# Optimization experiments

Hardware: AMD Instinct MI355X
Metric: run time of the kernel (lower is better)

## Reference

```python
import jax, jax.numpy as jnp
import numpy as np

THRESH = 8000.0  # saturating partial-sum accumulator threshold (thresh=8000 in source)
GROUP = 128      # channel chunk size used by split_tensor_* helpers
EPS = 1e-5

def binarize(x):
    # sign() forward with straight-through estimator (standard BinarizeConv2d behavior)
    return x + jax.lax.stop_gradient(jnp.sign(x) - x)

def psum_conv3x3(x, w):
    """3x3 'same' conv computed as 9 shifted-window partial sums per 128-channel
    group, with the running accumulator saturated to [-THRESH, THRESH] after each
    partial sum (emulating a low-bit hardware accumulator).
    x: [B, C, H, W]; w: [O, C, 3, 3] -> out [B, O, H, W]."""
    B, C, H, W = x.shape
    O = w.shape[0]
    xp = jnp.pad(x, ((0, 0), (0, 0), (1, 1), (1, 1)))
    acc = jnp.zeros((B, O, H, W), dtype=x.dtype)
    n_groups = C // GROUP
    for g in range(n_groups):
        xg = xp[:, g * GROUP:(g + 1) * GROUP]
        wg = w[:, g * GROUP:(g + 1) * GROUP]
        # split_tensor ordering: x1..x9 vary row (dim2) fastest, then col (dim3)
        for col in range(3):
            for row in range(3):
                part = jnp.einsum('bchw,oc->bohw',
                                  xg[:, :, row:row + H, col:col + W],
                                  wg[:, :, row, col])
                acc = jnp.clip(acc + part, -THRESH, THRESH)
    return acc

def batchnorm(x, gamma, beta, mean, var):
    inv = gamma / jnp.sqrt(var + EPS)
    return x * inv[None, :, None, None] + (beta - mean * inv)[None, :, None, None]

def setup_inputs() -> dict:
    key = jax.random.key(0)
    ks = jax.random.split(key, 12)
    B, C, H, W = 64, 128, 56, 56
    return {
        'x': jax.random.normal(ks[0], (B, C, H, W), jnp.float32),
        'w1': jax.random.normal(ks[1], (C, C, 3, 3), jnp.float32),
        'w2': jax.random.normal(ks[2], (C, C, 3, 3), jnp.float32),
        'gamma1': jax.random.uniform(ks[3], (C,), jnp.float32, 0.5, 1.5),
        'beta1': jax.random.normal(ks[4], (C,), jnp.float32) * 0.1,
        'mean1': jax.random.normal(ks[5], (C,), jnp.float32),
        'var1': jax.random.uniform(ks[6], (C,), jnp.float32, 0.5, 1.5),
        'gamma2': jax.random.uniform(ks[7], (C,), jnp.float32, 0.5, 1.5),
        'beta2': jax.random.normal(ks[8], (C,), jnp.float32) * 0.1,
        'mean2': jax.random.normal(ks[9], (C,), jnp.float32),
        'var2': jax.random.uniform(ks[10], (C,), jnp.float32, 0.5, 1.5),
    }

def reference(x, w1, w2, gamma1, beta1, mean1, var1, gamma2, beta2, mean2, var2):
    residual = x
    out = psum_conv3x3(binarize(x), binarize(w1))
    out = batchnorm(out, gamma1, beta1, mean1, var1)
    out = jnp.clip(out, -1.0, 1.0)  # hardtanh
    out = psum_conv3x3(binarize(out), binarize(w2))
    out = batchnorm(out, gamma2, beta2, mean2, var2)
    out = out + residual
    out = jnp.clip(out, -1.0, 1.0)
    return out
```

## Files before the change

### kernel.cpp

```cpp
#include <hip/hip_runtime.h>
#include <cstdint>
#include <cstddef>


typedef int      v4i __attribute__((ext_vector_type(4)));
typedef float    v4f __attribute__((ext_vector_type(4)));

constexpr int B = 64, C = 128, H = 56, W = 56;
constexpr int HP = H + 2, WP = W + 2;
constexpr int PIX = H * W;
constexpr int M = B * H * W;
constexpr int NTILES = M / 256;
constexpr int TPX = NTILES / 8;

constexpr size_t XS_BYTES = (size_t)B * HP * WP * C;
constexpr size_t XS1_OFF = 0;
constexpr size_t XS2_OFF = XS_BYTES;
constexpr size_t WF_BYTES = 18 * 8192;
constexpr size_t WF1_OFF = 2 * XS_BYTES;
constexpr size_t WF2_OFF = WF1_OFF + WF_BYTES;
constexpr size_t BNP_OFF = WF2_OFF + WF_BYTES;

__global__ __launch_bounds__(256) void zero_halo(int8_t* __restrict__ xs1,
                                                 int8_t* __restrict__ xs2) {
    int b = blockIdx.x >> 2;
    int q = blockIdx.x & 3;
    int t = q * 256 + threadIdx.x;
    size_t ib = (size_t)b * HP * WP * C;
#pragma unroll
    for (int a = 0; a < 2; ++a) {
        uint32_t* p = (uint32_t*)((a ? xs2 : xs1) + ib);
        const int ROWD = WP * C / 4;
        for (int i = t; i < ROWD; i += 1024) {
            p[i] = 0;
            p[(HP - 1) * ROWD + i] = 0;
        }
        for (int i = t; i < 56 * 2 * 32; i += 1024) {
            int r = i >> 6;
            int side = (i >> 5) & 1;
            int j = i & 31;
            p[((r + 1) * WP + side * (WP - 1)) * (C / 4) + j] = 0;
        }
    }
}

__global__ __launch_bounds__(256) void prep_x(const float* __restrict__ x,
                                              int8_t* __restrict__ xs) {
    __shared__ uint32_t tl[256 * 33];
    int t = threadIdx.x;
    int m = blockIdx.x * 256 + t;
    int b_ = m / PIX, hw = m % PIX;
    const float* xp = x + (size_t)b_ * C * PIX + hw;
#pragma unroll
    for (int c4 = 0; c4 < 32; ++c4) {
        uint32_t v = 0;
#pragma unroll
        for (int j = 0; j < 4; ++j) {
            float f = xp[(size_t)(c4 * 4 + j) * PIX];
            v |= ((uint32_t)(uint8_t)(int8_t)((f > 0.f) - (f < 0.f))) << (8 * j);
        }
        tl[t * 33 + c4] = v;
    }
    __syncthreads();
    int pl = t >> 3, co = t & 7;
#pragma unroll
    for (int pass = 0; pass < 8; ++pass) {
        int p = pass * 32 + pl;
        int mg = blockIdx.x * 256 + p;
        int b2 = mg / PIX, hw2 = mg % PIX, h2 = hw2 / W, w2 = hw2 % W;
        size_t ob = ((size_t)(b2 * HP + h2 + 1) * WP + (w2 + 1)) * C + co * 16;
        v4i val;
#pragma unroll
        for (int k = 0; k < 4; ++k) val[k] = (int)tl[p * 33 + co * 4 + k];
        *(v4i*)(xs + ob) = val;
    }
}

__global__ __launch_bounds__(256) void prep_w(
    const float* __restrict__ w1, const float* __restrict__ w2,
    const float* __restrict__ g1, const float* __restrict__ be1,
    const float* __restrict__ mu1, const float* __restrict__ va1,
    const float* __restrict__ g2, const float* __restrict__ be2,
    const float* __restrict__ mu2, const float* __restrict__ va2,
    int8_t* __restrict__ wf1, int8_t* __restrict__ wf2,
    float* __restrict__ bnp) {
    int t = blockIdx.x * 256 + threadIdx.x;
    if (t < 256) {
        int o = t & 127;
        if (t < 128) {
            float inv = g1[o] / sqrtf(va1[o] + 1e-5f);
            bnp[o]       = inv;
            bnp[128 + o] = __fsub_rn(be1[o], __fmul_rn(mu1[o], inv));
        } else {
            float inv = g2[o] / sqrtf(va2[o] + 1e-5f);
            bnp[256 + o] = inv;
            bnp[384 + o] = __fsub_rn(be2[o], __fmul_rn(mu2[o], inv));
        }
    }
    if (t >= 2 * 18 * 8 * 64) return;
    int lane = t & 63;
    int j    = (t >> 6) & 7;
    int kh   = (t >> 9) & 1;
    int tap  = (t >> 10) % 9;
    int which = (t >> 10) / 9;
    const float* w = which ? w2 : w1;
    int8_t* wf = which ? wf2 : wf1;
    int o = (j >> 2) * 64 + (lane & 15) * 4 + (j & 3);
    int cbase = kh * 64 + (lane >> 4) * 16;
    int r = tap / 3, s = tap % 3;
    int8_t frag[16];
#pragma unroll
    for (int jj = 0; jj < 16; ++jj) {
        float f = w[((size_t)(o * C + cbase + jj) * 3 + r) * 3 + s];
        frag[jj] = (int8_t)((f > 0.f) - (f < 0.f));
    }
    *(v4i*)(wf + (size_t)(((tap * 2 + kh) * 8 + j) * 64 + lane) * 16) =
        *(const v4i*)frag;
}

template <int PHASE>
__global__ __launch_bounds__(512, 1) void conv_bin(
    const int8_t* __restrict__ xs,
    const int8_t* __restrict__ wf,
    const float* __restrict__ bnp,
    const float* __restrict__ xres,
    int8_t* __restrict__ xs_next,
    float* __restrict__ out)
{
    __shared__ int8_t wlds[18 * 8192];
    int t = threadIdx.x, lane = t & 63, wv = t >> 6;
    int quad = lane >> 4, l15 = lane & 15;
    int wrow  = wv & 3;
    int whalf = wv >> 2;

    {
        const v4i* g = (const v4i*)wf;
        v4i* l = (v4i*)wlds;
        for (int i = t; i < 18 * 512; i += 512) l[i] = g[i];
    }
    float binv[4], btt[4];
    int obase = whalf * 64 + l15 * 4;
    {
        int o0 = (PHASE == 1 ? 0 : 256) + obase;
        int o1 = (PHASE == 1 ? 128 : 384) + obase;
#pragma unroll
        for (int nl = 0; nl < 4; ++nl) { binv[nl] = bnp[o0 + nl]; btt[nl] = bnp[o1 + nl]; }
    }
    __syncthreads();

    int xcd = blockIdx.x & 7, local = blockIdx.x >> 3;
#pragma unroll 1
    for (int tloc = local; tloc < TPX; tloc += 32) {
        int tile = xcd * TPX + tloc;
        int mwave = tile * 256 + wrow * 64;
        int abase[4];
#pragma unroll
        for (int rg = 0; rg < 4; ++rg) {
            int ma = mwave + rg * 16 + l15;
            int wa = ma % W; int ta = ma / W; int ha = ta % H; int ba = ta / H;
            abase[rg] = ((ba * HP + ha) * WP + wa) * C + quad * 16;
        }

        v4i acc[4][4];
#pragma unroll
        for (int rg = 0; rg < 4; ++rg)
#pragma unroll
            for (int nl = 0; nl < 4; ++nl) acc[rg][nl] = (v4i)0;

        v4i a[4];
#pragma unroll
        for (int rg = 0; rg < 4; ++rg) a[rg] = *(const v4i*)(xs + abase[rg]);

#pragma unroll 1
        for (int step = 0; step < 18; ++step) {
            v4i an[4];
            if (step + 1 < 18) {
                int nt = (step + 1) >> 1, nk = (step + 1) & 1;
                int aoff = ((nt / 3) * WP + (nt % 3)) * C + nk * 64;
#pragma unroll
                for (int rg = 0; rg < 4; ++rg)
                    an[rg] = *(const v4i*)(xs + abase[rg] + aoff);
            }
            const int8_t* lb = wlds + step * 8192 + whalf * 4096;
#pragma unroll
            for (int nl = 0; nl < 4; ++nl) {
                v4i bf = *(const v4i*)(lb + ((nl * 64 + lane) << 4));
#pragma unroll
                for (int rg = 0; rg < 4; ++rg)
                    acc[rg][nl] = __builtin_amdgcn_mfma_i32_16x16x64_i8(
                        a[rg], bf, acc[rg][nl], 0, 0, 0);
            }
#pragma unroll
            for (int rg = 0; rg < 4; ++rg) a[rg] = an[rg];
        }

#pragma unroll
        for (int rg = 0; rg < 4; ++rg) {
            int m0 = mwave + rg * 16 + quad * 4;
            int w0 = m0 % W; int t0 = m0 / W; int h0 = t0 % H; int b0 = t0 / H;
            if (PHASE == 1) {
                int base = ((b0 * HP + h0 + 1) * WP + (w0 + 1)) * C + obase;
#pragma unroll
                for (int i = 0; i < 4; ++i) {
                    uint32_t pk = 0;
#pragma unroll
                    for (int nl = 0; nl < 4; ++nl) {
                        float y = __fadd_rn(__fmul_rn((float)acc[rg][nl][i], binv[nl]), btt[nl]);
                        pk |= ((uint32_t)(uint8_t)(int8_t)((y > 0.f) - (y < 0.f))) << (8 * nl);
                    }
                    *(uint32_t*)(xs_next + base + i * C) = pk;
                }
            } else {
                int pixb = b0 * C * PIX + h0 * W + w0;
#pragma unroll
                for (int nl = 0; nl < 4; ++nl) {
                    int idx = pixb + (obase + nl) * PIX;
                    v4f r = *(const v4f*)(xres + idx);
                    v4f z;
#pragma unroll
                    for (int i = 0; i < 4; ++i) {
                        float y = __fadd_rn(__fmul_rn((float)acc[rg][nl][i], binv[nl]), btt[nl]);
                        float v = __fadd_rn(y, r[i]);
                        z[i] = fminf(fmaxf(v, -1.f), 1.f);
                    }
                    *(v4f*)(out + idx) = z;
                }
            }
        }
    }
}

extern "C" void kernel_launch(void* const* d_in, const int* in_sizes, int n_in,
                              void* d_out, int out_size, void* d_ws, size_t ws_size,
                              hipStream_t stream) {
    const float* x   = (const float*)d_in[0];
    const float* w1  = (const float*)d_in[1];
    const float* w2  = (const float*)d_in[2];
    const float* g1  = (const float*)d_in[3];
    const float* be1 = (const float*)d_in[4];
    const float* mu1 = (const float*)d_in[5];
    const float* va1 = (const float*)d_in[6];
    const float* g2  = (const float*)d_in[7];
    const float* be2 = (const float*)d_in[8];
    const float* mu2 = (const float*)d_in[9];
    const float* va2 = (const float*)d_in[10];

    int8_t* ws  = (int8_t*)d_ws;
    int8_t* xs1 = ws + XS1_OFF;
    int8_t* xs2 = ws + XS2_OFF;
    int8_t* wf1 = ws + WF1_OFF;
    int8_t* wf2 = ws + WF2_OFF;
    float*  bnp = (float*)(ws + BNP_OFF);

    zero_halo<<<256, 256, 0, stream>>>(xs1, xs2);
    prep_x<<<M / 256, 256, 0, stream>>>(x, xs1);
    prep_w<<<(2 * 18 * 8 * 64 + 255) / 256, 256, 0, stream>>>(
        w1, w2, g1, be1, mu1, va1, g2, be2, mu2, va2, wf1, wf2, bnp);

    conv_bin<1><<<256, 512, 0, stream>>>(xs1, wf1, bnp, nullptr, xs2, nullptr);
    conv_bin<2><<<256, 512, 0, stream>>>(xs2, wf2, bnp, x, nullptr, (float*)d_out);
}
```

Baseline: 397.1 us.

## Double conv block to 1024 threads, shrink per-wave tile, prefetch LDS weights

The conv kernels now launch 1024 threads per block with 16 waves, each covering 32 pixel rows instead of 64, so twice as many waves share the same LDS weight copy. This hides latency through more waves rather than more per-wave work. Weight fragments for the next step are prefetched from LDS into registers alongside the next activation loads. Nontemporal loads are added for the fp32 input reads in prep_x and the residual reads. Each B fragment is now reused by only 2 MFMAs instead of 4, which raises LDS traffic per MFMA.

```diff
diff --git a/kernel.cpp b/kernel.cpp
--- a/kernel.cpp
+++ b/kernel.cpp
@@ -56,7 +56,7 @@
         uint32_t v = 0;
 #pragma unroll
         for (int j = 0; j < 4; ++j) {
-            float f = xp[(size_t)(c4 * 4 + j) * PIX];
+            float f = __builtin_nontemporal_load(xp + (size_t)(c4 * 4 + j) * PIX);
             v |= ((uint32_t)(uint8_t)(int8_t)((f > 0.f) - (f < 0.f))) << (8 * j);
         }
         tl[t * 33 + c4] = v;
@@ -119,7 +119,7 @@
 }
 
 template <int PHASE>
-__global__ __launch_bounds__(512, 1) void conv_bin(
+__global__ __launch_bounds__(1024, 1) void conv_bin(
     const int8_t* __restrict__ xs,
     const int8_t* __restrict__ wf,
     const float* __restrict__ bnp,
@@ -130,13 +130,13 @@
     __shared__ int8_t wlds[18 * 8192];
     int t = threadIdx.x, lane = t & 63, wv = t >> 6;
     int quad = lane >> 4, l15 = lane & 15;
-    int wrow  = wv & 3;
-    int whalf = wv >> 2;
+    int wrow  = wv & 7;
+    int whalf = wv >> 3;
 
     {
         const v4i* g = (const v4i*)wf;
         v4i* l = (v4i*)wlds;
-        for (int i = t; i < 18 * 512; i += 512) l[i] = g[i];
+        for (int i = t; i < 18 * 512; i += 1024) l[i] = g[i];
     }
     float binv[4], btt[4];
     int obase = whalf * 64 + l15 * 4;
@@ -152,50 +152,61 @@
 #pragma unroll 1
     for (int tloc = local; tloc < TPX; tloc += 32) {
         int tile = xcd * TPX + tloc;
-        int mwave = tile * 256 + wrow * 64;
-        int abase[4];
-#pragma unroll
-        for (int rg = 0; rg < 4; ++rg) {
+        int mwave = tile * 256 + wrow * 32;
+        int abase[2];
+#pragma unroll
+        for (int rg = 0; rg < 2; ++rg) {
             int ma = mwave + rg * 16 + l15;
             int wa = ma % W; int ta = ma / W; int ha = ta % H; int ba = ta / H;
             abase[rg] = ((ba * HP + ha) * WP + wa) * C + quad * 16;
         }
 
-        v4i acc[4][4];
-#pragma unroll
-        for (int rg = 0; rg < 4; ++rg)
+        v4i acc[2][4];
+#pragma unroll
+        for (int rg = 0; rg < 2; ++rg)
 #pragma unroll
             for (int nl = 0; nl < 4; ++nl) acc[rg][nl] = (v4i)0;
 
-        v4i a[4];
-#pragma unroll
-        for (int rg = 0; rg < 4; ++rg) a[rg] = *(const v4i*)(xs + abase[rg]);
+        v4i a[2], bf[4];
+#pragma unroll
+        for (int rg = 0; rg < 2; ++rg) a[rg] = *(const v4i*)(xs + abase[rg]);
+        {
+            const int8_t* lb = wlds + whalf * 4096;
+#pragma unroll
+            for (int nl = 0; nl < 4; ++nl)
+                bf[nl] = *(const v4i*)(lb + ((nl * 64 + lane) << 4));
+        }
 
 #pragma unroll 1
         for (int step = 0; step < 18; ++step) {
-            v4i an[4];
+            v4i an[2], bfn[4];
             if (step + 1 < 18) {
-                int nt = (step + 1) >> 1, nk = (step + 1) & 1;
-                int aoff = ((nt / 3) * WP + (nt % 3)) * C + nk * 64;
-#pragma unroll
-                for (int rg = 0; rg < 4; ++rg)
+                int nt_ = (step + 1) >> 1, nk = (step + 1) & 1;
+                int aoff = ((nt_ / 3) * WP + (nt_ % 3)) * C + nk * 64;
+#pragma unroll
+                for (int rg = 0; rg < 2; ++rg)
                     an[rg] = *(const v4i*)(xs + abase[rg] + aoff);
+                const int8_t* lbn = wlds + (step + 1) * 8192 + whalf * 4096;
+#pragma unroll
+                for (int nl = 0; nl < 4; ++nl)
+                    bfn[nl] = *(const v4i*)(lbn + ((nl * 64 + lane) << 4));
             }
-            const int8_t* lb = wlds + step * 8192 + whalf * 4096;
-#pragma unroll
-            for (int nl = 0; nl < 4; ++nl) {
-                v4i bf = *(const v4i*)(lb + ((nl * 64 + lane) << 4));
-#pragma unroll
-                for (int rg = 0; rg < 4; ++rg)
+#pragma unroll
+            for (int nl = 0; nl < 4; ++nl)
+#pragma unroll
+                for (int rg = 0; rg < 2; ++rg)
                     acc[rg][nl] = __builtin_amdgcn_mfma_i32_16x16x64_i8(
-                        a[rg], bf, acc[rg][nl], 0, 0, 0);
+                        a[rg], bf[nl], acc[rg][nl], 0, 0, 0);
+            if (step + 1 < 18) {
+#pragma unroll
+                for (int rg = 0; rg < 2; ++rg) a[rg] = an[rg];
+#pragma unroll
+                for (int nl = 0; nl < 4; ++nl) bf[nl] = bfn[nl];
             }
-#pragma unroll
-            for (int rg = 0; rg < 4; ++rg) a[rg] = an[rg];
-        }
-
-#pragma unroll
-        for (int rg = 0; rg < 4; ++rg) {
+        }
+
+#pragma unroll
+        for (int rg = 0; rg < 2; ++rg) {
             int m0 = mwave + rg * 16 + quad * 4;
             int w0 = m0 % W; int t0 = m0 / W; int h0 = t0 % H; int b0 = t0 / H;
             if (PHASE == 1) {
@@ -215,7 +226,7 @@
 #pragma unroll
                 for (int nl = 0; nl < 4; ++nl) {
                     int idx = pixb + (obase + nl) * PIX;
-                    v4f r = *(const v4f*)(xres + idx);
+                    v4f r = __builtin_nontemporal_load((const v4f*)(xres + idx));
                     v4f z;
 #pragma unroll
                     for (int i = 0; i < 4; ++i) {
@@ -257,6 +268,6 @@
     prep_w<<<(2 * 18 * 8 * 64 + 255) / 256, 256, 0, stream>>>(
         w1, w2, g1, be1, mu1, va1, g2, be2, mu2, va2, wf1, wf2, bnp);
 
-    conv_bin<1><<<256, 512, 0, stream>>>(xs1, wf1, bnp, nullptr, xs2, nullptr);
-    conv_bin<2><<<256, 512, 0, stream>>>(xs2, wf2, bnp, x, nullptr, (float*)d_out);
-}
+    conv_bin<1><<<256, 1024, 0, stream>>>(xs1, wf1, bnp, nullptr, xs2, nullptr);
+    conv_bin<2><<<256, 1024, 0, stream>>>(xs2, wf2, bnp, x, nullptr, (float*)d_out);
+}
```

Result: no change. 394.6 us (-0.6%).
